# Kernel optimization log

Measured on AMD Instinct MI355X. Metric: run time of the kernel, lower is better.

## Reference

```python
import jax, jax.numpy as jnp
import numpy as np

D_MODEL = 2048
N_HEADS = 16
D_K = D_MODEL // N_HEADS
D_FF = ((int(D_MODEL * 8 / 3) + 63) // 64) * 64  # 5504
B, S = 2, 2048
EPS = 1e-6


def setup_inputs() -> dict:
    key = jax.random.key(0)
    ks = jax.random.split(key, 16)
    sc = 0.02
    x = jax.random.normal(ks[0], (B, S, D_MODEL), dtype=jnp.float32)
    mask = jnp.tril(jnp.ones((S, S), dtype=jnp.int32))[None]  # [1,S,S] causal
    inp = {
        'x': x,
        'mask': mask,
        'wq': jax.random.normal(ks[1], (D_MODEL, D_MODEL), jnp.float32) * sc,
        'bq': jnp.zeros((D_MODEL,), jnp.float32),
        'wk': jax.random.normal(ks[2], (D_MODEL, D_MODEL), jnp.float32) * sc,
        'bk': jnp.zeros((D_MODEL,), jnp.float32),
        'wv': jax.random.normal(ks[3], (D_MODEL, D_MODEL), jnp.float32) * sc,
        'bv': jnp.zeros((D_MODEL,), jnp.float32),
        'wo': jax.random.normal(ks[4], (D_MODEL, D_MODEL), jnp.float32) * sc,
        'bo': jnp.zeros((D_MODEL,), jnp.float32),
        'g1': jnp.ones((D_MODEL,), jnp.float32),  # RMSNorm weights
        'g2': jnp.ones((D_MODEL,), jnp.float32),
        'w1': jax.random.normal(ks[5], (D_MODEL, D_FF), jnp.float32) * sc,
        'w3': jax.random.normal(ks[6], (D_MODEL, D_FF), jnp.float32) * sc,
        'w2': jax.random.normal(ks[7], (D_FF, D_MODEL), jnp.float32) * sc,
    }
    return inp


def _rmsnorm(x, w):
    rms = jnp.sqrt(jnp.mean(x * x, axis=-1, keepdims=True) + EPS)
    return x / rms * w


def _block(x, mask, wq, bq, wk, bk, wv, bv, wo, bo, g1, g2, w1, w2, w3):
    b, s, _ = x.shape
    # --- attention sublayer (pre-LN) ---
    n = _rmsnorm(x, g1)
    q = (n @ wq + bq).reshape(b, s, N_HEADS, D_K).transpose(0, 2, 1, 3)
    k = (n @ wk + bk).reshape(b, s, N_HEADS, D_K).transpose(0, 2, 1, 3)
    v = (n @ wv + bv).reshape(b, s, N_HEADS, D_K).transpose(0, 2, 1, 3)
    scores = jnp.einsum('bhqd,bhkd->bhqk', q, k) / jnp.sqrt(jnp.float32(D_K))
    m = mask[:, None, :, :]  # [1,1,S,S]
    scores = jnp.where(m == 0, jnp.float32(-jnp.inf), scores)
    attn = jax.nn.softmax(scores, axis=-1)
    ao = jnp.einsum('bhqk,bhkd->bhqd', attn, v)
    ao = ao.transpose(0, 2, 1, 3).reshape(b, s, D_MODEL)
    x = x + (ao @ wo + bo)
    # --- SwiGLU FFN sublayer (pre-LN) ---
    n = _rmsnorm(x, g2)
    ffn = (jax.nn.silu(n @ w1) * (n @ w3)) @ w2
    return x + ffn


def reference(x, mask, wq, bq, wk, bk, wv, bv, wo, bo, g1, g2, w1, w2, w3):
    return _block(x, mask, wq, bq, wk, bk, wv, bv, wo, bo, g1, g2, w1, w2, w3)
```

## Files before the change

kernel.cpp:

```cpp
#include <hip/hip_runtime.h>
#include <stdint.h>

typedef unsigned short u16;
typedef __bf16 bf16x8 __attribute__((ext_vector_type(8)));
typedef float f32x4 __attribute__((ext_vector_type(4)));

#define D_MODEL 2048
#define NHEADS 16
#define DK 128
#define DFF 5504
#define DFFP 5632
#define BB 2
#define SS 2048
#define MTOK 4096
#define DQKV 6144

#define AS1 __attribute__((address_space(1)))
#define AS3 __attribute__((address_space(3)))

__device__ __forceinline__ u16 f2bf(float f){
  union { float f; uint32_t u; } v; v.f = f;
  uint32_t r = v.u + 0x7fffu + ((v.u >> 16) & 1u);
  return (u16)(r >> 16);
}
__device__ __forceinline__ float bf2f(u16 u){
  union { uint32_t u; float f; } v; v.u = ((uint32_t)u) << 16;
  return v.f;
}
__device__ __forceinline__ u16 cvt_bf16(float f){
  union { __bf16 h; u16 u; } v; v.h = (__bf16)f; return v.u;
}
__device__ __forceinline__ float fexp2(float x){
#if __has_builtin(__builtin_amdgcn_exp2f)
  return __builtin_amdgcn_exp2f(x);
#else
  return exp2f(x);
#endif
}

__global__ __launch_bounds__(256) void k_transpose_w(const float* __restrict__ W,
                                                     u16* __restrict__ Wt, int K, int Nsrc){
  __shared__ float tile[32][33];
  int n0 = blockIdx.x * 32, k0 = blockIdx.y * 32;
  int tx = threadIdx.x, ty = threadIdx.y;
  #pragma unroll
  for (int r = 0; r < 4; ++r){
    int n = n0 + tx;
    tile[ty + r*8][tx] = (n < Nsrc) ? W[(size_t)(k0 + ty + r*8) * Nsrc + n] : 0.0f;
  }
  __syncthreads();
  #pragma unroll
  for (int r = 0; r < 4; ++r)
    Wt[(size_t)(n0 + ty + r*8) * K + k0 + tx] = f2bf(tile[tx][ty + r*8]);
}

__global__ __launch_bounds__(256) void k_transpose_w4(
    const float* __restrict__ w0s, const float* __restrict__ w1s,
    const float* __restrict__ w2s, const float* __restrict__ w3s,
    u16* __restrict__ d0, u16* __restrict__ d1,
    u16* __restrict__ d2, u16* __restrict__ d3){
  __shared__ float tile[32][33];
  const float* W = blockIdx.z == 0 ? w0s : blockIdx.z == 1 ? w1s : blockIdx.z == 2 ? w2s : w3s;
  u16* Wt = blockIdx.z == 0 ? d0 : blockIdx.z == 1 ? d1 : blockIdx.z == 2 ? d2 : d3;
  int n0 = blockIdx.x * 32, k0 = blockIdx.y * 32;
  int tx = threadIdx.x, ty = threadIdx.y;
  #pragma unroll
  for (int r = 0; r < 4; ++r)
    tile[ty + r*8][tx] = W[(size_t)(k0 + ty + r*8) * D_MODEL + n0 + tx];
  __syncthreads();
  #pragma unroll
  for (int r = 0; r < 4; ++r)
    Wt[(size_t)(n0 + ty + r*8) * D_MODEL + k0 + tx] = f2bf(tile[tx][ty + r*8]);
}

__global__ __launch_bounds__(256) void k_transpose_v(const u16* __restrict__ V,
                                                     u16* __restrict__ Vt, int ld){
  __shared__ u16 tile[32][33];
  int s0 = blockIdx.x * 32;
  int bh = blockIdx.y >> 2, dt = blockIdx.y & 3;
  int b = bh >> 4, h = bh & 15;
  int tx = threadIdx.x, ty = threadIdx.y;
  #pragma unroll
  for (int r = 0; r < 4; ++r)
    tile[ty + r*8][tx] = V[(size_t)(b*SS + s0 + ty + r*8) * ld + h*DK + dt*32 + tx];
  __syncthreads();
  #pragma unroll
  for (int r = 0; r < 4; ++r)
    Vt[(size_t)(bh*DK + dt*32 + ty + r*8) * SS + s0 + tx] = tile[tx][ty + r*8];
}

__global__ __launch_bounds__(256) void k_concat3(const float* __restrict__ a,
                                                 const float* __restrict__ b,
                                                 const float* __restrict__ c,
                                                 float* __restrict__ o){
  int i = blockIdx.x*256 + threadIdx.x;
  if (i >= DQKV) return;
  o[i] = (i < 2048) ? a[i] : (i < 4096 ? b[i-2048] : c[i-4096]);
}

__global__ __launch_bounds__(256) void k_rmsnorm(const float* __restrict__ X,
                                                 const float* __restrict__ g,
                                                 u16* __restrict__ out){
  int row = blockIdx.x, tid = threadIdx.x;
  const float* x = X + (size_t)row * D_MODEL;
  float4 a = ((const float4*)x)[tid*2];
  float4 b = ((const float4*)x)[tid*2+1];
  float ss = a.x*a.x + a.y*a.y + a.z*a.z + a.w*a.w
           + b.x*b.x + b.y*b.y + b.z*b.z + b.w*b.w;
  #pragma unroll
  for (int m = 1; m < 64; m <<= 1) ss += __shfl_xor(ss, m, 64);
  __shared__ float red[4];
  if ((tid & 63) == 0) red[tid >> 6] = ss;
  __syncthreads();
  float tot = red[0] + red[1] + red[2] + red[3];
  float sc = rsqrtf(tot * (1.0f / D_MODEL) + 1e-6f);
  float4 ga = ((const float4*)g)[tid*2];
  float4 gb = ((const float4*)g)[tid*2+1];
  uint32_t w0 = f2bf(a.x*sc*ga.x) | ((uint32_t)f2bf(a.y*sc*ga.y) << 16);
  uint32_t w1 = f2bf(a.z*sc*ga.z) | ((uint32_t)f2bf(a.w*sc*ga.w) << 16);
  uint32_t w2 = f2bf(b.x*sc*gb.x) | ((uint32_t)f2bf(b.y*sc*gb.y) << 16);
  uint32_t w3 = f2bf(b.z*sc*gb.z) | ((uint32_t)f2bf(b.w*sc*gb.w) << 16);
  ((uint4*)(out + (size_t)row * D_MODEL))[tid] = make_uint4(w0, w1, w2, w3);
}

__global__ __launch_bounds__(256) void k_silu_mul(const u16* __restrict__ a,
                                                  const u16* __restrict__ b,
                                                  u16* __restrict__ o, int n8){
  int i = blockIdx.x * 256 + threadIdx.x;
  if (i >= n8) return;
  uint4 av = ((const uint4*)a)[i];
  uint4 bv = ((const uint4*)b)[i];
  uint32_t aa[4] = {av.x, av.y, av.z, av.w};
  uint32_t bb[4] = {bv.x, bv.y, bv.z, bv.w};
  uint32_t rr[4];
  #pragma unroll
  for (int j = 0; j < 4; ++j){
    float x0 = bf2f((u16)(aa[j] & 0xffff)), x1 = bf2f((u16)(aa[j] >> 16));
    float y0 = bf2f((u16)(bb[j] & 0xffff)), y1 = bf2f((u16)(bb[j] >> 16));
    float r0 = x0 / (1.f + __expf(-x0)) * y0;
    float r1 = x1 / (1.f + __expf(-x1)) * y1;
    rr[j] = f2bf(r0) | ((uint32_t)f2bf(r1) << 16);
  }
  ((uint4*)o)[i] = make_uint4(rr[0], rr[1], rr[2], rr[3]);
}

__global__ __launch_bounds__(256) void k_add2(float* __restrict__ out,
                                              const float* __restrict__ p0,
                                              const float* __restrict__ p1, int n4){
  int stride = gridDim.x * 256;
  for (int i = blockIdx.x * 256 + threadIdx.x; i < n4; i += stride){
    float4 o = ((const float4*)out)[i];
    float4 a = ((const float4*)p0)[i];
    float4 b = ((const float4*)p1)[i];
    o.x += a.x + b.x; o.y += a.y + b.y; o.z += a.z + b.z; o.w += a.w + b.w;
    ((float4*)out)[i] = o;
  }
}

__global__ __launch_bounds__(256) void k_addres(float* __restrict__ out,
                                                const float* __restrict__ x,
                                                const float* __restrict__ bias,
                                                const float* __restrict__ p0,
                                                const float* __restrict__ p1, int n4){
  int stride = gridDim.x * 256;
  for (int i = blockIdx.x * 256 + threadIdx.x; i < n4; i += stride){
    float4 o = ((const float4*)x)[i];
    float4 bb = ((const float4*)bias)[i & (D_MODEL/4 - 1)];
    float4 a = ((const float4*)p0)[i];
    float4 b = ((const float4*)p1)[i];
    o.x += bb.x + a.x + b.x; o.y += bb.y + a.y + b.y;
    o.z += bb.z + a.z + b.z; o.w += bb.w + a.w + b.w;
    ((float4*)out)[i] = o;
  }
}

template<int EPI>
__global__ __launch_bounds__(512, 2) void k_gemm8p(
    const u16* __restrict__ A, const u16* __restrict__ Bt,
    const float* __restrict__ bias, const u16* __restrict__ aux,
    void* __restrict__ Cout, int M, int N, int K,
    int lda, int ldb, int ldc)
{
  extern __shared__ __align__(16) char smem[];
  const int tid = threadIdx.x;
  const int lane = tid & 63, wid = tid >> 6;
  const int wr = wid >> 2, wc = wid & 3;
  const int lrow = lane & 15, lhi = lane >> 4;

  int nwg = gridDim.x, wg = blockIdx.x;
  int ksl = 0;
  if constexpr (EPI == 6){
    int hn = nwg >> 1;
    if (wg >= hn){ ksl = 1; wg -= hn; }
    nwg = hn;
    A  += (size_t)ksl * K;
    Bt += (size_t)ksl * K;
  }

  int nbx = N >> 8, nbm = M >> 8;
  int xcd = wg & 7, sub = wg >> 3;
  int m0, n0;
  if ((nwg & 7) == 0 && (nbm & 1) == 0 && (nbx & 3) == 0){
    int mh = nbm >> 1;
    int mr = sub % mh, nc = sub / mh;
    m0 = (((xcd & 1) * mh) + mr) << 8;
    n0 = (((xcd >> 1) * (nbx >> 2)) + nc) << 8;
  } else {
    int qq = nwg >> 3, rr2 = nwg & 7;
    int swz = (xcd < rr2 ? xcd*(qq+1) : rr2*(qq+1) + (xcd-rr2)*qq) + sub;
    m0 = (swz / nbx) << 8; n0 = (swz % nbx) << 8;
  }

  const int nk = K >> 6;
  const int hA = wr, hB = wc >> 1;
  const int gA = wc;
  const int gB = (wr << 1) | (wc & 1);

  const u16* aSrc[2][2]; int aDst[2][2];
  const u16* bSrc[2][2]; int bDst[2][2];
  #pragma unroll
  for (int q = 0; q < 2; ++q)
    #pragma unroll
    for (int L = 0; L < 2; ++L){
      int p = q*8192 + gA*2048 + L*1024 + lane*16;
      int row = p >> 7;
      int o = (p & 127) ^ ((row & 7) << 4);
      aSrc[q][L] = A + (size_t)(m0 + hA*128 + row)*lda + (o >> 1);
      aDst[q][L] = hA*16384 + p;
      int pb = q*4096 + (gB >> 1)*8192 + (gB & 1)*2048 + L*1024 + lane*16;
      int rowb = pb >> 7;
      int ob = (pb & 127) ^ ((rowb & 7) << 4);
      bSrc[q][L] = Bt + (size_t)(n0 + hB*128 + rowb)*ldb + (ob >> 1);
      bDst[q][L] = 32768 + hB*16384 + pb;
    }
  const int xo0 = (lhi*16) ^ ((lrow & 7) << 4);
  const int xo1 = (64 + lhi*16) ^ ((lrow & 7) << 4);

  auto stA = [&](int d, int kk, int q){
    #pragma unroll
    for (int L = 0; L < 2; ++L)
      __builtin_amdgcn_global_load_lds(
        (const AS1 void*)(aSrc[q][L] + kk),
        (AS3 void*)(smem + d*65536 + aDst[q][L]), 16, 0, 0);
  };
  auto stB = [&](int d, int kk, int s){
    #pragma unroll
    for (int L = 0; L < 2; ++L)
      __builtin_amdgcn_global_load_lds(
        (const AS1 void*)(bSrc[s][L] + kk),
        (AS3 void*)(smem + d*65536 + bDst[s][L]), 16, 0, 0);
  };
  auto rdA = [&](int d, int rloc, int ks)->bf16x8{
    return *(const bf16x8*)(smem + d*65536 + hA*16384 + rloc*128 + (ks ? xo1 : xo0));
  };
  auto rdB = [&](int d, int rloc, int ks)->bf16x8{
    return *(const bf16x8*)(smem + d*65536 + 32768 + hB*16384 + rloc*128 + (ks ? xo1 : xo0));
  };

  f32x4 acc[8][4] = {};

  stA(0, 0, 0); stB(0, 0, 0); stB(0, 0, 1); stA(0, 0, 1);
  asm volatile("s_waitcnt vmcnt(0)" ::: "memory");
  __builtin_amdgcn_s_barrier();

  for (int t = 0; t < nk; ++t){
    int d = t & 1, dn = d ^ 1, kkn = (t + 1) << 6;
    bool pf = (t + 1 < nk);
    bf16x8 aR[8], bQ0[4], bQ1[4];

    #pragma unroll
    for (int ii = 0; ii < 4; ++ii){
      aR[ii*2]   = rdA(d, ii*16 + lrow, 0);
      aR[ii*2+1] = rdA(d, ii*16 + lrow, 1);
    }
    #pragma unroll
    for (int j = 0; j < 2; ++j){
      bQ0[j*2]   = rdB(d, (wc&1)*64 + j*16 + lrow, 0);
      bQ0[j*2+1] = rdB(d, (wc&1)*64 + j*16 + lrow, 1);
    }
    if (pf){ stA(dn, kkn, 0); stB(dn, kkn, 0); }
    __builtin_amdgcn_s_barrier();
    asm volatile("s_waitcnt lgkmcnt(0)" ::: "memory");
    __builtin_amdgcn_sched_barrier(0);
    __builtin_amdgcn_s_setprio(1);
    #pragma unroll
    for (int ii = 0; ii < 4; ++ii)
      #pragma unroll
      for (int j = 0; j < 2; ++j){
        acc[ii][j] = __builtin_amdgcn_mfma_f32_16x16x32_bf16(aR[ii*2],   bQ0[j*2],   acc[ii][j], 0, 0, 0);
        acc[ii][j] = __builtin_amdgcn_mfma_f32_16x16x32_bf16(aR[ii*2+1], bQ0[j*2+1], acc[ii][j], 0, 0, 0);
      }
    __builtin_amdgcn_s_setprio(0);
    if (pf) asm volatile("s_waitcnt vmcnt(6)" ::: "memory");
    else    asm volatile("s_waitcnt vmcnt(2)" ::: "memory");
    __builtin_amdgcn_sched_barrier(0);
    __builtin_amdgcn_s_barrier();

    #pragma unroll
    for (int j = 0; j < 2; ++j){
      bQ1[j*2]   = rdB(d, (wc&1)*64 + 32 + j*16 + lrow, 0);
      bQ1[j*2+1] = rdB(d, (wc&1)*64 + 32 + j*16 + lrow, 1);
    }
    if (pf) stB(dn, kkn, 1);
    __builtin_amdgcn_s_barrier();
    asm volatile("s_waitcnt lgkmcnt(0)" ::: "memory");
    __builtin_amdgcn_sched_barrier(0);
    __builtin_amdgcn_s_setprio(1);
    #pragma unroll
    for (int ii = 0; ii < 4; ++ii)
      #pragma unroll
      for (int j = 0; j < 2; ++j){
        acc[ii][2+j] = __builtin_amdgcn_mfma_f32_16x16x32_bf16(aR[ii*2],   bQ1[j*2],   acc[ii][2+j], 0, 0, 0);
        acc[ii][2+j] = __builtin_amdgcn_mfma_f32_16x16x32_bf16(aR[ii*2+1], bQ1[j*2+1], acc[ii][2+j], 0, 0, 0);
      }
    __builtin_amdgcn_s_setprio(0);
    if (pf) asm volatile("s_waitcnt vmcnt(6)" ::: "memory");
    else    asm volatile("s_waitcnt vmcnt(0)" ::: "memory");
    __builtin_amdgcn_sched_barrier(0);
    __builtin_amdgcn_s_barrier();

    #pragma unroll
    for (int ii = 0; ii < 4; ++ii){
      aR[ii*2]   = rdA(d, 64 + ii*16 + lrow, 0);
      aR[ii*2+1] = rdA(d, 64 + ii*16 + lrow, 1);
    }
    if (pf) stA(dn, kkn, 1);
    __builtin_amdgcn_s_barrier();
    asm volatile("s_waitcnt lgkmcnt(0)" ::: "memory");
    __builtin_amdgcn_sched_barrier(0);
    __builtin_amdgcn_s_setprio(1);
    #pragma unroll
    for (int ii = 0; ii < 4; ++ii)
      #pragma unroll
      for (int j = 0; j < 2; ++j){
        acc[4+ii][2+j] = __builtin_amdgcn_mfma_f32_16x16x32_bf16(aR[ii*2],   bQ1[j*2],   acc[4+ii][2+j], 0, 0, 0);
        acc[4+ii][2+j] = __builtin_amdgcn_mfma_f32_16x16x32_bf16(aR[ii*2+1], bQ1[j*2+1], acc[4+ii][2+j], 0, 0, 0);
      }
    __builtin_amdgcn_s_setprio(0);
    __builtin_amdgcn_s_barrier();

    __builtin_amdgcn_s_setprio(1);
    #pragma unroll
    for (int ii = 0; ii < 4; ++ii)
      #pragma unroll
      for (int j = 0; j < 2; ++j){
        acc[4+ii][j] = __builtin_amdgcn_mfma_f32_16x16x32_bf16(aR[ii*2],   bQ0[j*2],   acc[4+ii][j], 0, 0, 0);
        acc[4+ii][j] = __builtin_amdgcn_mfma_f32_16x16x32_bf16(aR[ii*2+1], bQ0[j*2+1], acc[4+ii][j], 0, 0, 0);
      }
    __builtin_amdgcn_s_setprio(0);
    if (pf) asm volatile("s_waitcnt vmcnt(4)" ::: "memory");
    __builtin_amdgcn_sched_barrier(0);
    __builtin_amdgcn_s_barrier();
  }

  if constexpr (EPI == 6){
    float* P = ksl ? (float*)aux : (float*)Cout;
    #pragma unroll
    for (int i = 0; i < 8; ++i)
      #pragma unroll
      for (int j = 0; j < 4; ++j){
        int col = n0 + wc*64 + j*16 + lrow;
        #pragma unroll
        for (int q = 0; q < 4; ++q){
          int row = m0 + wr*128 + i*16 + lhi*4 + q;
          P[(size_t)row*ldc + col] = acc[i][j][q];
        }
      }
    return;
  }
  u16* Cw = (u16*)Cout;
  int cofs = 0;
  if constexpr (EPI == 5){
    if (n0 >= 5632){ Cw = (u16*)aux; cofs = 5632; }
  }
  #pragma unroll
  for (int i = 0; i < 8; ++i){
    #pragma unroll
    for (int j = 0; j < 4; ++j){
      int col = n0 + wc*64 + j*16 + lrow;
      float bv = 0.f;
      if constexpr (EPI == 0) bv = bias[col];
      #pragma unroll
      for (int q = 0; q < 4; ++q){
        int row = m0 + wr*128 + i*16 + lhi*4 + q;
        float v = acc[i][j][q] + bv;
        Cw[(size_t)row*ldc + (col - cofs)] = f2bf(v);
      }
    }
  }
}

template<int EPI>
__global__ __launch_bounds__(256) void k_gemm_bt(
    const u16* __restrict__ A, const u16* __restrict__ Bt,
    const float* __restrict__ bias, const float* __restrict__ res,
    const u16* __restrict__ aux,
    void* __restrict__ Cout, int M, int N, int K,
    int lda, int ldb, int ldc)
{
  __shared__ __align__(16) u16 As[3][128*32];
  __shared__ __align__(16) u16 Bs[3][128*32];
  int tid = threadIdx.x;

  int nwg = gridDim.x, wg = blockIdx.x;
  int qq = nwg >> 3, rr = nwg & 7;
  int xcd = wg & 7, sub = wg >> 3;
  int swz = (xcd < rr ? xcd*(qq+1) : rr*(qq+1) + (xcd-rr)*qq) + sub;
  int nbx = N >> 7;
  int m0 = (swz / nbx) << 7, n0 = (swz % nbx) << 7;

  int lane = tid & 63, wave = tid >> 6;
  int wr = wave >> 1, wc = wave & 1;
  int lrow = lane & 15, lhi = lane >> 4;
  f32x4 acc[4][4] = {};
  int srow = tid >> 2;
  int schk = tid & 3;
  const int nk = K >> 5;

  auto stage = [&](int slot, int kt){
    int k0 = kt << 5;
    int c = schk ^ (srow & 3);
    #pragma unroll
    for (int cc = 0; cc < 2; ++cc){
      int r = cc*64 + srow;
      __builtin_amdgcn_global_load_lds(
        (const AS1 void*)(A + (size_t)(m0 + r)*lda + k0 + c*8),
        (AS3 void*)(&As[slot][r*32 + schk*8]), 16, 0, 0);
      __builtin_amdgcn_global_load_lds(
        (const AS1 void*)(Bt + (size_t)(n0 + r)*ldb + k0 + c*8),
        (AS3 void*)(&Bs[slot][r*32 + schk*8]), 16, 0, 0);
    }
  };

  stage(0, 0);
  if (nk > 1) stage(1, 1);
  if (nk > 1) asm volatile("s_waitcnt vmcnt(4)" ::: "memory");
  else        asm volatile("s_waitcnt vmcnt(0)" ::: "memory");
  __builtin_amdgcn_s_barrier();

  for (int kt = 0; kt < nk; ++kt){
    int cur = kt % 3;
    if (kt + 2 < nk) stage((kt + 2) % 3, kt + 2);
    int rchk = lhi ^ (lrow & 3);
    bf16x8 af[4], bfv[4];
    #pragma unroll
    for (int i = 0; i < 4; ++i){
      af[i]  = *(const bf16x8*)(&As[cur][(wr*64 + i*16 + lrow)*32 + rchk*8]);
      bfv[i] = *(const bf16x8*)(&Bs[cur][(wc*64 + i*16 + lrow)*32 + rchk*8]);
    }
    #pragma unroll
    for (int i = 0; i < 4; ++i)
      #pragma unroll
      for (int j = 0; j < 4; ++j)
        acc[i][j] = __builtin_amdgcn_mfma_f32_16x16x32_bf16(af[i], bfv[j], acc[i][j], 0, 0, 0);
    if (kt + 2 < nk) asm volatile("s_waitcnt vmcnt(4)" ::: "memory");
    else             asm volatile("s_waitcnt vmcnt(0)" ::: "memory");
    __builtin_amdgcn_s_barrier();
  }

  #pragma unroll
  for (int i = 0; i < 4; ++i){
    #pragma unroll
    for (int j = 0; j < 4; ++j){
      int col = n0 + wc*64 + j*16 + lrow;
      float bv = 0.f;
      if constexpr (EPI == 0 || EPI == 1) bv = bias[col];
      #pragma unroll
      for (int q = 0; q < 4; ++q){
        int row = m0 + wr*64 + i*16 + lhi*4 + q;
        size_t idx = (size_t)row*ldc + col;
        float v = acc[i][j][q] + bv;
        if constexpr (EPI == 1 || EPI == 3) v += res[idx];
        if constexpr (EPI == 4){
          float a0 = bf2f(aux[idx]);
          v = a0 / (1.f + __expf(-a0)) * v;
        }
        if constexpr (EPI == 0 || EPI == 2 || EPI == 4) ((u16*)Cout)[idx] = f2bf(v);
        else ((float*)Cout)[idx] = v;
      }
    }
  }
}

__global__ __launch_bounds__(512) void k_attn(
    const u16* __restrict__ Q, const u16* __restrict__ Kb,
    const u16* __restrict__ Vt, u16* __restrict__ O, int ldq)
{
  int tid = threadIdx.x, lane = tid & 63, wave = tid >> 6;
  int lrow = lane & 15, lhi = lane >> 4;
  int bidx = blockIdx.x;
  int bh = bidx >> 3, j = bidx & 7;
  int b = bh >> 4, h = bh & 15;

  __shared__ __align__(16) u16 Kbuf[2][64*128];
  __shared__ __align__(16) u16 Vbuf[2][128*64];
  __shared__ __align__(16) u16 P_lds[8][16*64];
  char* pw = (char*)&P_lds[wave][0];
  const float sc2 = 0.08838834764831845f * 1.44269504088896340736f;

  auto stage = [&](int bufi, int kt){
    int kv0 = kt << 6;
    char* kd = (char*)&Kbuf[bufi][0];
    char* vd = (char*)&Vbuf[bufi][0];
    #pragma unroll
    for (int L = 0; L < 2; ++L){
      int cid = wave*128 + L*64 + lane;
      int r = cid >> 4, c = cid & 15;
      int cg = c ^ (r & 7);
      __builtin_amdgcn_global_load_lds(
        (const AS1 void*)(Kb + (size_t)(b*SS + kv0 + r)*ldq + h*DK + cg*8),
        (AS3 void*)(kd + wave*2048 + L*1024 + lane*16), 16, 0, 0);
      int dd = cid >> 3, c8 = cid & 7;
      int cv = c8 ^ (dd & 7);
      __builtin_amdgcn_global_load_lds(
        (const AS1 void*)(Vt + (size_t)bh*DK*SS + (size_t)dd*SS + kv0 + cv*8),
        (AS3 void*)(vd + wave*2048 + L*1024 + lane*16), 16, 0, 0);
    }
  };

  #pragma unroll 1
  for (int item = 0; item < 2; ++item){
    int qi = item == 0 ? 15 - j : j;
    int qs = qi * 128;
    int nt = 2*qi + 2;
    int qrow = qs + wave * 16;

    bf16x8 qf[4];
    const u16* qbase = Q + (size_t)(b*SS + qrow + lrow)*ldq + h*DK + lhi*8;
    #pragma unroll
    for (int dc = 0; dc < 4; ++dc) qf[dc] = *(const bf16x8*)(qbase + dc*32);

    f32x4 accO[8] = {};
    float mr[4] = {-1e30f,-1e30f,-1e30f,-1e30f};
    float lr[4] = {0.f,0.f,0.f,0.f};

    stage(0, 0);
    __syncthreads();

    for (int kt = 0; kt < nt; ++kt){
      int cur = kt & 1;
      if (kt + 1 < nt) stage(cur ^ 1, kt + 1);
      int kv0 = kt << 6;
      if (kv0 <= qrow + 15){
        const char* kl = (const char*)&Kbuf[cur][0];
        const char* vl = (const char*)&Vbuf[cur][0];
        bool domask = (kv0 + 63 > qrow);

        f32x4 sf[4];
        #pragma unroll
        for (int hf = 0; hf < 4; ++hf){
          int rl = hf*16 + lrow;
          int sw = rl & 7;
          f32x4 a = {};
          #pragma unroll
          for (int dc = 0; dc < 4; ++dc){
            bf16x8 kf = *(const bf16x8*)(kl + rl*256 + (((lhi + dc*4) ^ sw) << 4));
            a = __builtin_amdgcn_mfma_f32_16x16x32_bf16(qf[dc], kf, a, 0, 0, 0);
          }
          sf[hf] = a;
        }

        float p[4][4], mx[4];
        #pragma unroll
        for (int q = 0; q < 4; ++q){
          float s0 = sf[0][q]*sc2, s1 = sf[1][q]*sc2, s2 = sf[2][q]*sc2, s3 = sf[3][q]*sc2;
          if (domask){
            int qg = qrow + lhi*4 + q;
            if (kv0      + lrow > qg) s0 = -1e30f;
            if (kv0 + 16 + lrow > qg) s1 = -1e30f;
            if (kv0 + 32 + lrow > qg) s2 = -1e30f;
            if (kv0 + 48 + lrow > qg) s3 = -1e30f;
          }
          p[q][0]=s0; p[q][1]=s1; p[q][2]=s2; p[q][3]=s3;
          float m = fmaxf(fmaxf(s0,s1), fmaxf(s2,s3));
          m = fmaxf(m, __shfl_xor(m, 1, 64));
          m = fmaxf(m, __shfl_xor(m, 2, 64));
          m = fmaxf(m, __shfl_xor(m, 4, 64));
          m = fmaxf(m, __shfl_xor(m, 8, 64));
          mx[q] = m;
        }
        float dmax = fmaxf(fmaxf(mx[0]-mr[0], mx[1]-mr[1]), fmaxf(mx[2]-mr[2], mx[3]-mr[3]));
        bool rescale = !__all(dmax <= 8.0f);
        float al[4];
        #pragma unroll
        for (int q = 0; q < 4; ++q){
          if (rescale){
            float mn = fmaxf(mr[q], mx[q]);
            al[q] = fexp2(mr[q] - mn);
            mr[q] = mn;
          } else al[q] = 1.0f;
          p[q][0] = fexp2(p[q][0] - mr[q]);
          p[q][1] = fexp2(p[q][1] - mr[q]);
          p[q][2] = fexp2(p[q][2] - mr[q]);
          p[q][3] = fexp2(p[q][3] - mr[q]);
          float sm = (p[q][0] + p[q][1]) + (p[q][2] + p[q][3]);
          sm += __shfl_xor(sm, 1, 64);
          sm += __shfl_xor(sm, 2, 64);
          sm += __shfl_xor(sm, 4, 64);
          sm += __shfl_xor(sm, 8, 64);
          lr[q] = lr[q]*al[q] + sm;
        }
        if (rescale){
          #pragma unroll
          for (int f = 0; f < 8; ++f)
            #pragma unroll
            for (int q = 0; q < 4; ++q) accO[f][q] *= al[q];
        }

        #pragma unroll
        for (int q = 0; q < 4; ++q){
          int row = lhi*4 + q;
          int rb = row*128, sw = (row & 7) << 4;
          #pragma unroll
          for (int hf = 0; hf < 4; ++hf)
            *(u16*)(pw + rb + ((hf*32 + lrow*2) ^ sw)) = cvt_bf16(p[q][hf]);
        }
        __builtin_amdgcn_sched_barrier(0);
        int rsw = (lrow & 7) << 4;
        bf16x8 pa0 = *(const bf16x8*)(pw + lrow*128 + ((     lhi*16) ^ rsw));
        bf16x8 pa1 = *(const bf16x8*)(pw + lrow*128 + ((64 + lhi*16) ^ rsw));

        #pragma unroll
        for (int f = 0; f < 8; ++f){
          int d = f*16 + lrow;
          int swv = d & 7;
          bf16x8 v0 = *(const bf16x8*)(vl + d*128 + (((lhi    ) ^ swv) << 4));
          bf16x8 v1 = *(const bf16x8*)(vl + d*128 + (((lhi + 4) ^ swv) << 4));
          accO[f] = __builtin_amdgcn_mfma_f32_16x16x32_bf16(pa0, v0, accO[f], 0, 0, 0);
          accO[f] = __builtin_amdgcn_mfma_f32_16x16x32_bf16(pa1, v1, accO[f], 0, 0, 0);
        }
      }
      __syncthreads();
    }

    #pragma unroll
    for (int q = 0; q < 4; ++q){
      float inv = 1.0f / lr[q];
      #pragma unroll
      for (int f = 0; f < 8; ++f){
        int row = b*SS + qrow + lhi*4 + q;
        int col = h*DK + f*16 + lrow;
        O[(size_t)row*D_MODEL + col] = cvt_bf16(accO[f][q] * inv);
      }
    }
    __syncthreads();
  }
}

extern "C" void kernel_launch(void* const* d_in, const int* in_sizes, int n_in,
                              void* d_out, int out_size, void* d_ws, size_t ws_size,
                              hipStream_t stream)
{
  (void)in_sizes; (void)n_in; (void)out_size;
  const float* x  = (const float*)d_in[0];
  const float* wq = (const float*)d_in[2];
  const float* bq = (const float*)d_in[3];
  const float* wk = (const float*)d_in[4];
  const float* bk = (const float*)d_in[5];
  const float* wv = (const float*)d_in[6];
  const float* bv = (const float*)d_in[7];
  const float* wo = (const float*)d_in[8];
  const float* bo = (const float*)d_in[9];
  const float* g1 = (const float*)d_in[10];
  const float* g2 = (const float*)d_in[11];
  const float* w1 = (const float*)d_in[12];
  const float* w3 = (const float*)d_in[13];
  const float* w2 = (const float*)d_in[14];
  float* out = (float*)d_out;

  const size_t MB = 1u << 20;
  const size_t W2T_B = (size_t)D_MODEL * DFF * sizeof(u16);
  const size_t NEED = 152*MB + W2T_B + 32768;
  if (ws_size < NEED) return;
  char* ws = (char*)d_ws;
  u16* bufA  = (u16*)(ws + 0);
  u16* qkv   = (u16*)(ws + 16*MB);
  u16* h1    = qkv;
  u16* wqkvt = (u16*)(ws + 64*MB);
  u16* w1w3t = (u16*)(ws + 64*MB);
  u16* wot   = (u16*)(ws + 88*MB);
  u16* vtb   = (u16*)(ws + 96*MB);
  u16* h3    = (u16*)(ws + 108*MB);
  float* p0o = (float*)(ws + 16*MB);
  float* p1o = (float*)(ws + 108*MB);
  float* p0  = (float*)(ws + 64*MB);
  float* p1  = (float*)(ws + 96*MB);
  u16* w2t   = (u16*)(ws + 152*MB);
  float* bqkv = (float*)(ws + 152*MB + W2T_B);

  bool big = true;
  big &= hipFuncSetAttribute((const void*)k_gemm8p<0>, hipFuncAttributeMaxDynamicSharedMemorySize, 131072) == hipSuccess;
  big &= hipFuncSetAttribute((const void*)k_gemm8p<5>, hipFuncAttributeMaxDynamicSharedMemorySize, 131072) == hipSuccess;
  big &= hipFuncSetAttribute((const void*)k_gemm8p<6>, hipFuncAttributeMaxDynamicSharedMemorySize, 131072) == hipSuccess;

  dim3 tb(32, 8);
  k_transpose_w4<<<dim3(64,64,4), tb, 0, stream>>>(wq, wk, wv, wo,
      wqkvt, wqkvt + 2048*2048, wqkvt + 2*2048*2048, wot);
  k_transpose_w<<<dim3(64, DFF/32), tb, 0, stream>>>(w2, w2t, DFF, D_MODEL);
  k_concat3<<<24, 256, 0, stream>>>(bq, bk, bv, bqkv);

  k_rmsnorm<<<MTOK, 256, 0, stream>>>(x, g1, bufA);
  if (big){
    k_gemm8p<0><<<(MTOK/256)*(DQKV/256), 512, 131072, stream>>>(bufA, wqkvt, bqkv, nullptr, qkv, MTOK, DQKV, D_MODEL, D_MODEL, D_MODEL, DQKV);
    k_transpose_v<<<dim3(SS/32, 128), tb, 0, stream>>>(qkv + 4096, vtb, DQKV);
    k_transpose_w<<<dim3(DFFP/32, 64), tb, 0, stream>>>(w1, w1w3t, D_MODEL, DFF);
    k_attn<<<dim3(BB*NHEADS*8), 512, 0, stream>>>(qkv, qkv + 2048, vtb, bufA, DQKV);
    k_gemm8p<6><<<2*(MTOK/256)*(D_MODEL/256), 512, 131072, stream>>>(bufA, wot, nullptr, (const u16*)p1o, p0o, MTOK, D_MODEL, D_MODEL/2, D_MODEL, D_MODEL, D_MODEL);
    k_addres<<<2048, 256, 0, stream>>>(out, x, bo, p0o, p1o, MTOK*D_MODEL/4);
    k_transpose_w<<<dim3(DFFP/32, 64), tb, 0, stream>>>(w3, w1w3t + (size_t)DFFP*2048, D_MODEL, DFF);
    k_rmsnorm<<<MTOK, 256, 0, stream>>>(out, g2, bufA);
    k_gemm8p<5><<<(MTOK/256)*((2*DFFP)/256), 512, 131072, stream>>>(bufA, w1w3t, nullptr, h3, h1, MTOK, 2*DFFP, D_MODEL, D_MODEL, D_MODEL, DFFP);
    k_silu_mul<<<(MTOK*DFFP/8 + 255)/256, 256, 0, stream>>>(h1, h3, h1, MTOK*DFFP/8);
    k_gemm8p<6><<<2*(MTOK/256)*(D_MODEL/256), 512, 131072, stream>>>(h1, w2t, nullptr, (const u16*)p1, p0, MTOK, D_MODEL, DFF/2, DFFP, DFF, D_MODEL);
    k_add2<<<2048, 256, 0, stream>>>(out, p0, p1, MTOK*D_MODEL/4);
  } else {
    k_gemm_bt<0><<<(DQKV/128)*(MTOK/128), 256, 0, stream>>>(bufA, wqkvt, bqkv, nullptr, nullptr, qkv, MTOK, DQKV, D_MODEL, D_MODEL, D_MODEL, DQKV);
    k_transpose_v<<<dim3(SS/32, 128), tb, 0, stream>>>(qkv + 4096, vtb, DQKV);
    k_transpose_w<<<dim3(DFFP/32, 64), tb, 0, stream>>>(w1, w1w3t, D_MODEL, DFF);
    k_attn<<<dim3(BB*NHEADS*8), 512, 0, stream>>>(qkv, qkv + 2048, vtb, bufA, DQKV);
    k_gemm_bt<1><<<16*32, 256, 0, stream>>>(bufA, wot, bo, x, nullptr, out, MTOK, D_MODEL, D_MODEL, D_MODEL, D_MODEL, D_MODEL);
    k_transpose_w<<<dim3(DFFP/32, 64), tb, 0, stream>>>(w3, w1w3t + (size_t)DFFP*2048, D_MODEL, DFF);
    k_rmsnorm<<<MTOK, 256, 0, stream>>>(out, g2, bufA);
    k_gemm_bt<2><<<(DFFP/128)*32, 256, 0, stream>>>(bufA, w1w3t, nullptr, nullptr, nullptr, h1, MTOK, DFFP, D_MODEL, D_MODEL, D_MODEL, DFFP);
    k_gemm_bt<2><<<(DFFP/128)*32, 256, 0, stream>>>(bufA, w1w3t + (size_t)DFFP*2048, nullptr, nullptr, nullptr, h3, MTOK, DFFP, D_MODEL, D_MODEL, D_MODEL, DFFP);
    k_silu_mul<<<(MTOK*DFFP/8 + 255)/256, 256, 0, stream>>>(h1, h3, h1, MTOK*DFFP/8);
    k_gemm_bt<3><<<16*32, 256, 0, stream>>>(h1, w2t, nullptr, out, nullptr, out, MTOK, D_MODEL, DFF, DFFP, DFF, D_MODEL);
  }
}
```

Before: 675.4 us.

## Fuse residual add with RMSNorm, atomic split-K epilogue, merge w1/w3 transposes

Fuses the post-attention residual add (x + bias + split-K partials) with the second RMSNorm into one per-row kernel, saving a full round trip of the residual tensor. The FFN down-projection split-K GEMM now atomically adds its partials straight into the output, replacing the separate partial buffers and the add kernel. The w1 and w3 transposes are merged into one launch, and the GEMM main loop reorders its A/B global-to-LDS prefetch stages with adjusted vmcnt waits. The atomics add contention and make the summation order nondeterministic, and the reordered waits could expose latency.

Measured after the change: 686.8 us. No clear change (+1.7%).

```diff
diff --git a/kernel.cpp b/kernel.cpp
--- a/kernel.cpp
+++ b/kernel.cpp
@@ -67,6 +67,25 @@
   #pragma unroll
   for (int r = 0; r < 4; ++r)
     tile[ty + r*8][tx] = W[(size_t)(k0 + ty + r*8) * D_MODEL + n0 + tx];
+  __syncthreads();
+  #pragma unroll
+  for (int r = 0; r < 4; ++r)
+    Wt[(size_t)(n0 + ty + r*8) * D_MODEL + k0 + tx] = f2bf(tile[tx][ty + r*8]);
+}
+
+__global__ __launch_bounds__(256) void k_transpose_w13(
+    const float* __restrict__ w1s, const float* __restrict__ w3s,
+    u16* __restrict__ dst){
+  __shared__ float tile[32][33];
+  const float* W = blockIdx.z == 0 ? w1s : w3s;
+  u16* Wt = dst + (size_t)blockIdx.z * DFFP * D_MODEL;
+  int n0 = blockIdx.x * 32, k0 = blockIdx.y * 32;
+  int tx = threadIdx.x, ty = threadIdx.y;
+  #pragma unroll
+  for (int r = 0; r < 4; ++r){
+    int n = n0 + tx;
+    tile[ty + r*8][tx] = (n < DFF) ? W[(size_t)(k0 + ty + r*8) * DFF + n] : 0.0f;
+  }
   __syncthreads();
   #pragma unroll
   for (int r = 0; r < 4; ++r)
@@ -123,6 +142,45 @@
   ((uint4*)(out + (size_t)row * D_MODEL))[tid] = make_uint4(w0, w1, w2, w3);
 }
 
+__global__ __launch_bounds__(256) void k_addres_rms(
+    const float* __restrict__ X, const float* __restrict__ bias,
+    const float* __restrict__ p0, const float* __restrict__ p1,
+    const float* __restrict__ g, float* __restrict__ out,
+    u16* __restrict__ nrm){
+  int row = blockIdx.x, tid = threadIdx.x;
+  size_t base = (size_t)row * D_MODEL;
+  float4 a  = ((const float4*)(X  + base))[tid*2];
+  float4 b  = ((const float4*)(X  + base))[tid*2+1];
+  float4 ba = ((const float4*)bias)[tid*2];
+  float4 bb = ((const float4*)bias)[tid*2+1];
+  float4 pa = ((const float4*)(p0 + base))[tid*2];
+  float4 pb = ((const float4*)(p0 + base))[tid*2+1];
+  float4 qa = ((const float4*)(p1 + base))[tid*2];
+  float4 qb = ((const float4*)(p1 + base))[tid*2+1];
+  a.x += ba.x + pa.x + qa.x; a.y += ba.y + pa.y + qa.y;
+  a.z += ba.z + pa.z + qa.z; a.w += ba.w + pa.w + qa.w;
+  b.x += bb.x + pb.x + qb.x; b.y += bb.y + pb.y + qb.y;
+  b.z += bb.z + pb.z + qb.z; b.w += bb.w + pb.w + qb.w;
+  ((float4*)(out + base))[tid*2]   = a;
+  ((float4*)(out + base))[tid*2+1] = b;
+  float ss = a.x*a.x + a.y*a.y + a.z*a.z + a.w*a.w
+           + b.x*b.x + b.y*b.y + b.z*b.z + b.w*b.w;
+  #pragma unroll
+  for (int m = 1; m < 64; m <<= 1) ss += __shfl_xor(ss, m, 64);
+  __shared__ float red[4];
+  if ((tid & 63) == 0) red[tid >> 6] = ss;
+  __syncthreads();
+  float tot = red[0] + red[1] + red[2] + red[3];
+  float sc = rsqrtf(tot * (1.0f / D_MODEL) + 1e-6f);
+  float4 ga = ((const float4*)g)[tid*2];
+  float4 gb = ((const float4*)g)[tid*2+1];
+  uint32_t w0 = f2bf(a.x*sc*ga.x) | ((uint32_t)f2bf(a.y*sc*ga.y) << 16);
+  uint32_t w1 = f2bf(a.z*sc*ga.z) | ((uint32_t)f2bf(a.w*sc*ga.w) << 16);
+  uint32_t w2 = f2bf(b.x*sc*gb.x) | ((uint32_t)f2bf(b.y*sc*gb.y) << 16);
+  uint32_t w3 = f2bf(b.z*sc*gb.z) | ((uint32_t)f2bf(b.w*sc*gb.w) << 16);
+  ((uint4*)(nrm + base))[tid] = make_uint4(w0, w1, w2, w3);
+}
+
 __global__ __launch_bounds__(256) void k_silu_mul(const u16* __restrict__ a,
                                                   const u16* __restrict__ b,
                                                   u16* __restrict__ o, int n8){
@@ -142,36 +200,6 @@
     rr[j] = f2bf(r0) | ((uint32_t)f2bf(r1) << 16);
   }
   ((uint4*)o)[i] = make_uint4(rr[0], rr[1], rr[2], rr[3]);
-}
-
-__global__ __launch_bounds__(256) void k_add2(float* __restrict__ out,
-                                              const float* __restrict__ p0,
-                                              const float* __restrict__ p1, int n4){
-  int stride = gridDim.x * 256;
-  for (int i = blockIdx.x * 256 + threadIdx.x; i < n4; i += stride){
-    float4 o = ((const float4*)out)[i];
-    float4 a = ((const float4*)p0)[i];
-    float4 b = ((const float4*)p1)[i];
-    o.x += a.x + b.x; o.y += a.y + b.y; o.z += a.z + b.z; o.w += a.w + b.w;
-    ((float4*)out)[i] = o;
-  }
-}
-
-__global__ __launch_bounds__(256) void k_addres(float* __restrict__ out,
-                                                const float* __restrict__ x,
-                                                const float* __restrict__ bias,
-                                                const float* __restrict__ p0,
-                                                const float* __restrict__ p1, int n4){
-  int stride = gridDim.x * 256;
-  for (int i = blockIdx.x * 256 + threadIdx.x; i < n4; i += stride){
-    float4 o = ((const float4*)x)[i];
-    float4 bb = ((const float4*)bias)[i & (D_MODEL/4 - 1)];
-    float4 a = ((const float4*)p0)[i];
-    float4 b = ((const float4*)p1)[i];
-    o.x += bb.x + a.x + b.x; o.y += bb.y + a.y + b.y;
-    o.z += bb.z + a.z + b.z; o.w += bb.w + a.w + b.w;
-    ((float4*)out)[i] = o;
-  }
 }
 
 template<int EPI>
@@ -189,7 +217,7 @@
 
   int nwg = gridDim.x, wg = blockIdx.x;
   int ksl = 0;
-  if constexpr (EPI == 6){
+  if constexpr (EPI == 6 || EPI == 7){
     int hn = nwg >> 1;
     if (wg >= hn){ ksl = 1; wg -= hn; }
     nwg = hn;
@@ -278,7 +306,7 @@
       bQ0[j*2]   = rdB(d, (wc&1)*64 + j*16 + lrow, 0);
       bQ0[j*2+1] = rdB(d, (wc&1)*64 + j*16 + lrow, 1);
     }
-    if (pf){ stA(dn, kkn, 0); stB(dn, kkn, 0); }
+    if (pf) stA(dn, kkn, 0);
     __builtin_amdgcn_s_barrier();
     asm volatile("s_waitcnt lgkmcnt(0)" ::: "memory");
     __builtin_amdgcn_sched_barrier(0);
@@ -291,7 +319,7 @@
         acc[ii][j] = __builtin_amdgcn_mfma_f32_16x16x32_bf16(aR[ii*2+1], bQ0[j*2+1], acc[ii][j], 0, 0, 0);
       }
     __builtin_amdgcn_s_setprio(0);
-    if (pf) asm volatile("s_waitcnt vmcnt(6)" ::: "memory");
+    if (pf) asm volatile("s_waitcnt vmcnt(4)" ::: "memory");
     else    asm volatile("s_waitcnt vmcnt(2)" ::: "memory");
     __builtin_amdgcn_sched_barrier(0);
     __builtin_amdgcn_s_barrier();
@@ -300,6 +328,29 @@
     for (int j = 0; j < 2; ++j){
       bQ1[j*2]   = rdB(d, (wc&1)*64 + 32 + j*16 + lrow, 0);
       bQ1[j*2+1] = rdB(d, (wc&1)*64 + 32 + j*16 + lrow, 1);
+    }
+    if (pf) stB(dn, kkn, 0);
+    __builtin_amdgcn_s_barrier();
+    asm volatile("s_waitcnt lgkmcnt(0)" ::: "memory");
+    __builtin_amdgcn_sched_barrier(0);
+    __builtin_amdgcn_s_setprio(1);
+    #pragma unroll
+    for (int ii = 0; ii < 4; ++ii)
+      #pragma unroll
+      for (int j = 0; j < 2; ++j){
+        acc[ii][2+j] = __builtin_amdgcn_mfma_f32_16x16x32_bf16(aR[ii*2],   bQ1[j*2],   acc[ii][2+j], 0, 0, 0);
+        acc[ii][2+j] = __builtin_amdgcn_mfma_f32_16x16x32_bf16(aR[ii*2+1], bQ1[j*2+1], acc[ii][2+j], 0, 0, 0);
+      }
+    __builtin_amdgcn_s_setprio(0);
+    if (pf) asm volatile("s_waitcnt vmcnt(4)" ::: "memory");
+    else    asm volatile("s_waitcnt vmcnt(0)" ::: "memory");
+    __builtin_amdgcn_sched_barrier(0);
+    __builtin_amdgcn_s_barrier();
+
+    #pragma unroll
+    for (int ii = 0; ii < 4; ++ii){
+      aR[ii*2]   = rdA(d, 64 + ii*16 + lrow, 0);
+      aR[ii*2+1] = rdA(d, 64 + ii*16 + lrow, 1);
     }
     if (pf) stB(dn, kkn, 1);
     __builtin_amdgcn_s_barrier();
@@ -310,35 +361,13 @@
     for (int ii = 0; ii < 4; ++ii)
       #pragma unroll
       for (int j = 0; j < 2; ++j){
-        acc[ii][2+j] = __builtin_amdgcn_mfma_f32_16x16x32_bf16(aR[ii*2],   bQ1[j*2],   acc[ii][2+j], 0, 0, 0);
-        acc[ii][2+j] = __builtin_amdgcn_mfma_f32_16x16x32_bf16(aR[ii*2+1], bQ1[j*2+1], acc[ii][2+j], 0, 0, 0);
-      }
-    __builtin_amdgcn_s_setprio(0);
-    if (pf) asm volatile("s_waitcnt vmcnt(6)" ::: "memory");
-    else    asm volatile("s_waitcnt vmcnt(0)" ::: "memory");
-    __builtin_amdgcn_sched_barrier(0);
-    __builtin_amdgcn_s_barrier();
-
-    #pragma unroll
-    for (int ii = 0; ii < 4; ++ii){
-      aR[ii*2]   = rdA(d, 64 + ii*16 + lrow, 0);
-      aR[ii*2+1] = rdA(d, 64 + ii*16 + lrow, 1);
-    }
-    if (pf) stA(dn, kkn, 1);
-    __builtin_amdgcn_s_barrier();
-    asm volatile("s_waitcnt lgkmcnt(0)" ::: "memory");
-    __builtin_amdgcn_sched_barrier(0);
-    __builtin_amdgcn_s_setprio(1);
-    #pragma unroll
-    for (int ii = 0; ii < 4; ++ii)
-      #pragma unroll
-      for (int j = 0; j < 2; ++j){
         acc[4+ii][2+j] = __builtin_amdgcn_mfma_f32_16x16x32_bf16(aR[ii*2],   bQ1[j*2],   acc[4+ii][2+j], 0, 0, 0);
         acc[4+ii][2+j] = __builtin_amdgcn_mfma_f32_16x16x32_bf16(aR[ii*2+1], bQ1[j*2+1], acc[4+ii][2+j], 0, 0, 0);
       }
     __builtin_amdgcn_s_setprio(0);
     __builtin_amdgcn_s_barrier();
 
+    if (pf) stA(dn, kkn, 1);
     __builtin_amdgcn_s_setprio(1);
     #pragma unroll
     for (int ii = 0; ii < 4; ++ii)
@@ -364,6 +393,21 @@
         for (int q = 0; q < 4; ++q){
           int row = m0 + wr*128 + i*16 + lhi*4 + q;
           P[(size_t)row*ldc + col] = acc[i][j][q];
+        }
+      }
+    return;
+  }
+  if constexpr (EPI == 7){
+    float* P = (float*)Cout;
+    #pragma unroll
+    for (int i = 0; i < 8; ++i)
+      #pragma unroll
+      for (int j = 0; j < 4; ++j){
+        int col = n0 + wc*64 + j*16 + lrow;
+        #pragma unroll
+        for (int q = 0; q < 4; ++q){
+          int row = m0 + wr*128 + i*16 + lhi*4 + q;
+          atomicAdd(P + (size_t)row*ldc + col, acc[i][j][q]);
         }
       }
     return;
@@ -683,8 +727,6 @@
   u16* h3    = (u16*)(ws + 108*MB);
   float* p0o = (float*)(ws + 16*MB);
   float* p1o = (float*)(ws + 108*MB);
-  float* p0  = (float*)(ws + 64*MB);
-  float* p1  = (float*)(ws + 96*MB);
   u16* w2t   = (u16*)(ws + 152*MB);
   float* bqkv = (float*)(ws + 152*MB + W2T_B);
 
@@ -692,6 +734,7 @@
   big &= hipFuncSetAttribute((const void*)k_gemm8p<0>, hipFuncAttributeMaxDynamicSharedMemorySize, 131072) == hipSuccess;
   big &= hipFuncSetAttribute((const void*)k_gemm8p<5>, hipFuncAttributeMaxDynamicSharedMemorySize, 131072) == hipSuccess;
   big &= hipFuncSetAttribute((const void*)k_gemm8p<6>, hipFuncAttributeMaxDynamicSharedMemorySize, 131072) == hipSuccess;
+  big &= hipFuncSetAttribute((const void*)k_gemm8p<7>, hipFuncAttributeMaxDynamicSharedMemorySize, 131072) == hipSuccess;
 
   dim3 tb(32, 8);
   k_transpose_w4<<<dim3(64,64,4), tb, 0, stream>>>(wq, wk, wv, wo,
@@ -703,23 +746,19 @@
   if (big){
     k_gemm8p<0><<<(MTOK/256)*(DQKV/256), 512, 131072, stream>>>(bufA, wqkvt, bqkv, nullptr, qkv, MTOK, DQKV, D_MODEL, D_MODEL, D_MODEL, DQKV);
     k_transpose_v<<<dim3(SS/32, 128), tb, 0, stream>>>(qkv + 4096, vtb, DQKV);
-    k_transpose_w<<<dim3(DFFP/32, 64), tb, 0, stream>>>(w1, w1w3t, D_MODEL, DFF);
     k_attn<<<dim3(BB*NHEADS*8), 512, 0, stream>>>(qkv, qkv + 2048, vtb, bufA, DQKV);
     k_gemm8p<6><<<2*(MTOK/256)*(D_MODEL/256), 512, 131072, stream>>>(bufA, wot, nullptr, (const u16*)p1o, p0o, MTOK, D_MODEL, D_MODEL/2, D_MODEL, D_MODEL, D_MODEL);
-    k_addres<<<2048, 256, 0, stream>>>(out, x, bo, p0o, p1o, MTOK*D_MODEL/4);
-    k_transpose_w<<<dim3(DFFP/32, 64), tb, 0, stream>>>(w3, w1w3t + (size_t)DFFP*2048, D_MODEL, DFF);
-    k_rmsnorm<<<MTOK, 256, 0, stream>>>(out, g2, bufA);
+    k_transpose_w13<<<dim3(DFFP/32, 64, 2), tb, 0, stream>>>(w1, w3, w1w3t);
+    k_addres_rms<<<MTOK, 256, 0, stream>>>(x, bo, p0o, p1o, g2, out, bufA);
     k_gemm8p<5><<<(MTOK/256)*((2*DFFP)/256), 512, 131072, stream>>>(bufA, w1w3t, nullptr, h3, h1, MTOK, 2*DFFP, D_MODEL, D_MODEL, D_MODEL, DFFP);
     k_silu_mul<<<(MTOK*DFFP/8 + 255)/256, 256, 0, stream>>>(h1, h3, h1, MTOK*DFFP/8);
-    k_gemm8p<6><<<2*(MTOK/256)*(D_MODEL/256), 512, 131072, stream>>>(h1, w2t, nullptr, (const u16*)p1, p0, MTOK, D_MODEL, DFF/2, DFFP, DFF, D_MODEL);
-    k_add2<<<2048, 256, 0, stream>>>(out, p0, p1, MTOK*D_MODEL/4);
+    k_gemm8p<7><<<2*(MTOK/256)*(D_MODEL/256), 512, 131072, stream>>>(h1, w2t, nullptr, nullptr, out, MTOK, D_MODEL, DFF/2, DFFP, DFF, D_MODEL);
   } else {
     k_gemm_bt<0><<<(DQKV/128)*(MTOK/128), 256, 0, stream>>>(bufA, wqkvt, bqkv, nullptr, nullptr, qkv, MTOK, DQKV, D_MODEL, D_MODEL, D_MODEL, DQKV);
     k_transpose_v<<<dim3(SS/32, 128), tb, 0, stream>>>(qkv + 4096, vtb, DQKV);
-    k_transpose_w<<<dim3(DFFP/32, 64), tb, 0, stream>>>(w1, w1w3t, D_MODEL, DFF);
+    k_transpose_w13<<<dim3(DFFP/32, 64, 2), tb, 0, stream>>>(w1, w3, w1w3t);
     k_attn<<<dim3(BB*NHEADS*8), 512, 0, stream>>>(qkv, qkv + 2048, vtb, bufA, DQKV);
     k_gemm_bt<1><<<16*32, 256, 0, stream>>>(bufA, wot, bo, x, nullptr, out, MTOK, D_MODEL, D_MODEL, D_MODEL, D_MODEL, D_MODEL);
-    k_transpose_w<<<dim3(DFFP/32, 64), tb, 0, stream>>>(w3, w1w3t + (size_t)DFFP*2048, D_MODEL, DFF);
     k_rmsnorm<<<MTOK, 256, 0, stream>>>(out, g2, bufA);
     k_gemm_bt<2><<<(DFFP/128)*32, 256, 0, stream>>>(bufA, w1w3t, nullptr, nullptr, nullptr, h1, MTOK, DFFP, D_MODEL, D_MODEL, D_MODEL, DFFP);
     k_gemm_bt<2><<<(DFFP/128)*32, 256, 0, stream>>>(bufA, w1w3t + (size_t)DFFP*2048, nullptr, nullptr, nullptr, h3, MTOK, DFFP, D_MODEL, D_MODEL, D_MODEL, DFFP);
```
